# Performance work log

Hardware: AMD Instinct MI355X
Metric: run time of the kernel (lower is better)

The kernel has to match this reference:

```python
import jax, jax.numpy as jnp
import numpy as np

N_NODES = 100000
H_FEATS = 256
N_EDGES = 300000
NUM_CLASSES = 1


def setup_inputs() -> dict:
    key = jax.random.key(0)
    k1, k2, k3, k4, k5 = jax.random.split(key, 5)
    x = jax.random.normal(k1, (N_NODES, H_FEATS), dtype=jnp.float32)
    edge_index = jax.random.randint(k2, (2, N_EDGES), 0, N_NODES, dtype=jnp.int64)
    # MLP params (stored as [in, out] for x @ W + b)
    in1 = 2 * H_FEATS
    W1 = jax.random.normal(k3, (in1, H_FEATS), dtype=jnp.float32) / np.sqrt(in1)
    b1 = jnp.zeros((H_FEATS,), dtype=jnp.float32)
    W2 = jax.random.normal(k4, (H_FEATS, NUM_CLASSES), dtype=jnp.float32) / np.sqrt(H_FEATS)
    b2 = jnp.zeros((NUM_CLASSES,), dtype=jnp.float32)
    return {"x": x, "edge_index": edge_index, "W1": W1, "b1": b1, "W2": W2, "b2": b2}


def reference(x, edge_index, W1, b1, W2, b2):
    # Gather source/dest node embeddings and concat -> [E, 2*h_feats]
    h = jnp.concatenate([x[edge_index[0]], x[edge_index[1]]], axis=-1)
    h = jax.nn.relu(h @ W1 + b1)          # [E, h_feats]
    h = h @ W2 + b2                        # [E, num_classes]
    return jnp.squeeze(h, axis=1)          # [E]
```

## Files before the change

kernel.cpp:

```cpp
#include <hip/hip_runtime.h>
#include <hip/hip_bf16.h>

#define NN 100000
#define H  256
#define NE 300000
#define KOUT 512

typedef __attribute__((ext_vector_type(8))) short short8;
typedef __attribute__((ext_vector_type(8))) unsigned short ushort8v;
typedef __attribute__((ext_vector_type(4))) float f32x4;

__device__ __forceinline__ unsigned short f2bf(float f) {
    unsigned int u = __float_as_uint(f);
    u += 0x7FFFu + ((u >> 16) & 1u);
    return (unsigned short)(u >> 16);
}
__device__ __forceinline__ float bf2f(unsigned short h) {
    return __uint_as_float(((unsigned int)h) << 16);
}
__device__ __forceinline__ int swz(int row, int coloff) {
    return row * 128 + (coloff ^ ((row & 7) << 4));
}

__global__ __launch_bounds__(256) void wprep(const float* __restrict__ W1,
                                             unsigned short* __restrict__ wsB) {
    int gtid = blockIdx.x * 256 + threadIdx.x;
    int t  = gtid >> 10;
    int kg = (gtid >> 7) & 7;
    int n  = gtid & 127;
    int nt = t >> 2, ks = t & 3;
    int krow0 = ks * 64 + kg * 8 + ((nt >= 2) ? 256 : 0);
    int col = (nt & 1) * 128 + n;
    const float* src = W1 + (size_t)krow0 * 256 + col;
    ushort8v p;
    #pragma unroll
    for (int i = 0; i < 8; ++i) p[i] = f2bf(src[(size_t)i * 256]);
    *(ushort8v*)((char*)(wsB + t * 8192) + swz(n, kg * 16)) = p;
}

__global__ __launch_bounds__(256) void gemm_v2(const float* __restrict__ x,
                                               const unsigned short* __restrict__ wsB,
                                               unsigned short* __restrict__ y) {
    __shared__ unsigned short Al[128 * 64];
    __shared__ unsigned short Bl[128 * 64];
    const int tid = threadIdx.x;
    const int logical = ((int)blockIdx.x & 7) * ((int)gridDim.x >> 3) + ((int)blockIdx.x >> 3);
    const int mt = logical >> 2, nt = logical & 3;
    const int m0 = mt * 128;
    const int lane = tid & 63, wid = tid >> 6;
    const int wm = (wid >> 1) * 64, wn = (wid & 1) * 64;
    const int lr = lane & 15, lk = lane >> 4;

    const int arow = tid >> 2;
    const int acolb = (tid & 3) * 16;
    int r0 = m0 + arow;       if (r0 > NN - 1) r0 = NN - 1;
    int r1 = m0 + 64 + arow;  if (r1 > NN - 1) r1 = NN - 1;
    const float* xr0 = x + (size_t)r0 * H + acolb;
    const float* xr1 = x + (size_t)r1 * H + acolb;
    const unsigned short* bt = wsB + nt * 4 * 8192 + tid * 8;

    float4 pA[2][4];
    ushort8v pB[4];

    auto loadA = [&](int ks) {
        const float* s0 = xr0 + ks * 64;
        const float* s1 = xr1 + ks * 64;
        #pragma unroll
        for (int q = 0; q < 4; ++q) pA[0][q] = *(const float4*)(s0 + q * 4);
        #pragma unroll
        for (int q = 0; q < 4; ++q) pA[1][q] = *(const float4*)(s1 + q * 4);
    };
    auto loadB = [&](int ks) {
        const unsigned short* s = bt + ks * 8192;
        #pragma unroll
        for (int u = 0; u < 4; ++u) pB[u] = *(const ushort8v*)(s + u * 2048);
    };
    auto stage = [&]() {
        #pragma unroll
        for (int p = 0; p < 2; ++p) {
            int row = arow + p * 64;
            ushort8v q0, q1;
            q0[0]=f2bf(pA[p][0].x); q0[1]=f2bf(pA[p][0].y); q0[2]=f2bf(pA[p][0].z); q0[3]=f2bf(pA[p][0].w);
            q0[4]=f2bf(pA[p][1].x); q0[5]=f2bf(pA[p][1].y); q0[6]=f2bf(pA[p][1].z); q0[7]=f2bf(pA[p][1].w);
            q1[0]=f2bf(pA[p][2].x); q1[1]=f2bf(pA[p][2].y); q1[2]=f2bf(pA[p][2].z); q1[3]=f2bf(pA[p][2].w);
            q1[4]=f2bf(pA[p][3].x); q1[5]=f2bf(pA[p][3].y); q1[6]=f2bf(pA[p][3].z); q1[7]=f2bf(pA[p][3].w);
            *(ushort8v*)((char*)Al + swz(row, acolb * 2))      = q0;
            *(ushort8v*)((char*)Al + swz(row, acolb * 2 + 16)) = q1;
        }
        #pragma unroll
        for (int u = 0; u < 4; ++u) *(ushort8v*)(Bl + tid * 8 + u * 2048) = pB[u];
    };

    f32x4 acc[4][4] = {};
    loadA(0); loadB(0);
    #pragma unroll
    for (int ks = 0; ks < 4; ++ks) {
        stage();
        __syncthreads();
        if (ks < 3) { loadA(ks + 1); loadB(ks + 1); }
        #pragma unroll
        for (int kk = 0; kk < 64; kk += 32) {
            short8 a[4], b[4];
            const int coloff = kk * 2 + lk * 16;
            #pragma unroll
            for (int mi = 0; mi < 4; ++mi)
                a[mi] = *(const short8*)((const char*)Al + swz(wm + mi * 16 + lr, coloff));
            #pragma unroll
            for (int ni = 0; ni < 4; ++ni)
                b[ni] = *(const short8*)((const char*)Bl + swz(wn + ni * 16 + lr, coloff));
            #pragma unroll
            for (int mi = 0; mi < 4; ++mi)
                #pragma unroll
                for (int ni = 0; ni < 4; ++ni)
                    acc[mi][ni] = __builtin_amdgcn_mfma_f32_16x16x32_bf16(a[mi], b[ni], acc[mi][ni], 0, 0, 0);
        }
        if (ks < 3) {
            asm volatile("s_waitcnt lgkmcnt(0)" ::: "memory");
            __builtin_amdgcn_s_barrier();
            __builtin_amdgcn_sched_barrier(0);
        }
    }
    const int n0 = nt * 128;
    #pragma unroll
    for (int mi = 0; mi < 4; ++mi) {
        #pragma unroll
        for (int ni = 0; ni < 4; ++ni) {
            const int col = n0 + wn + ni * 16 + lr;
            #pragma unroll
            for (int r = 0; r < 4; ++r) {
                const int rowg = m0 + wm + mi * 16 + lk * 4 + r;
                if (rowg < NN) y[(size_t)rowg * KOUT + col] = f2bf(acc[mi][ni][r]);
            }
        }
    }
}

__global__ __launch_bounds__(256) void gemm_v1(const float* __restrict__ x,
                                               const float* __restrict__ W1,
                                               unsigned short* __restrict__ y) {
    __shared__ unsigned short Al[128 * 64];
    __shared__ unsigned short Bl[128 * 64];
    const int tid = threadIdx.x;
    const int bid = blockIdx.x;
    const int mt = bid >> 2, nt = bid & 3;
    const int m0 = mt * 128, n0 = nt * 128;
    const int lane = tid & 63, wid = tid >> 6;
    const int wm = (wid >> 1) * 64, wn = (wid & 1) * 64;
    const int lr = lane & 15, lk = lane >> 4;
    f32x4 acc[4][4] = {};
    for (int ks = 0; ks < 4; ++ks) {
        const int k0 = ks * 64;
        if (ks) __syncthreads();
        #pragma unroll
        for (int pass = 0; pass < 2; ++pass) {
            int f = pass * 4096 + tid * 16;
            int row = f >> 6, col = f & 63;
            int node = m0 + row;
            node = node < NN ? node : NN - 1;
            const float* src = x + (size_t)node * H + k0 + col;
            float4 v0 = *(const float4*)(src + 0);
            float4 v1 = *(const float4*)(src + 4);
            float4 v2 = *(const float4*)(src + 8);
            float4 v3 = *(const float4*)(src + 12);
            ushort8v p0, p1;
            p0[0]=f2bf(v0.x); p0[1]=f2bf(v0.y); p0[2]=f2bf(v0.z); p0[3]=f2bf(v0.w);
            p0[4]=f2bf(v1.x); p0[5]=f2bf(v1.y); p0[6]=f2bf(v1.z); p0[7]=f2bf(v1.w);
            p1[0]=f2bf(v2.x); p1[1]=f2bf(v2.y); p1[2]=f2bf(v2.z); p1[3]=f2bf(v2.w);
            p1[4]=f2bf(v3.x); p1[5]=f2bf(v3.y); p1[6]=f2bf(v3.z); p1[7]=f2bf(v3.w);
            *(ushort8v*)((char*)Al + swz(row, col * 2))      = p0;
            *(ushort8v*)((char*)Al + swz(row, col * 2 + 16)) = p1;
        }
        {
            int j  = tid & 127;
            int kh = tid >> 7;
            int rowbase = (n0 >= 256) ? 256 : 0;
            const float* wp = W1 + (size_t)(k0 + kh * 32 + rowbase) * 256 + (n0 & 255) + j;
            #pragma unroll
            for (int q = 0; q < 4; ++q) {
                ushort8v p;
                #pragma unroll
                for (int i = 0; i < 8; ++i) p[i] = f2bf(wp[(q * 8 + i) * 256]);
                *(ushort8v*)((char*)Bl + swz(j, (kh * 32 + q * 8) * 2)) = p;
            }
        }
        __syncthreads();
        #pragma unroll
        for (int kk = 0; kk < 64; kk += 32) {
            short8 a[4], b[4];
            const int coloff = kk * 2 + lk * 16;
            #pragma unroll
            for (int mi = 0; mi < 4; ++mi)
                a[mi] = *(const short8*)((const char*)Al + swz(wm + mi * 16 + lr, coloff));
            #pragma unroll
            for (int ni = 0; ni < 4; ++ni)
                b[ni] = *(const short8*)((const char*)Bl + swz(wn + ni * 16 + lr, coloff));
            #pragma unroll
            for (int mi = 0; mi < 4; ++mi)
                #pragma unroll
                for (int ni = 0; ni < 4; ++ni)
                    acc[mi][ni] = __builtin_amdgcn_mfma_f32_16x16x32_bf16(a[mi], b[ni], acc[mi][ni], 0, 0, 0);
        }
    }
    #pragma unroll
    for (int mi = 0; mi < 4; ++mi)
        #pragma unroll
        for (int ni = 0; ni < 4; ++ni) {
            const int col = n0 + wn + ni * 16 + lr;
            #pragma unroll
            for (int r = 0; r < 4; ++r) {
                const int rowg = m0 + wm + mi * 16 + lk * 4 + r;
                if (rowg < NN) y[(size_t)rowg * KOUT + col] = f2bf(acc[mi][ni][r]);
            }
        }
}

__global__ __launch_bounds__(256) void edge_v2(const unsigned short* __restrict__ y,
                                               const int* __restrict__ ei,
                                               const float* __restrict__ b1,
                                               const float* __restrict__ W2,
                                               const float* __restrict__ b2,
                                               float* __restrict__ out) {
    const int tid = threadIdx.x;
    const int l32 = tid & 31;
    const int ghw = ((int)(blockIdx.x * blockDim.x) + tid) >> 5;
    const int nhw = ((int)(gridDim.x * blockDim.x)) >> 5;
    const int j = l32 * 8;
    const float4 b01 = *(const float4*)(b1 + j);
    const float4 b23 = *(const float4*)(b1 + j + 4);
    const float4 w01 = *(const float4*)(W2 + j);
    const float4 w23 = *(const float4*)(W2 + j + 4);
    const float bb = b2[0];
    #pragma unroll 2
    for (int e = ghw; e < NE; e += nhw) {
        int s = ei[e], d = ei[NE + e];
        s = s < 0 ? 0 : (s > NN - 1 ? NN - 1 : s);
        d = d < 0 ? 0 : (d > NN - 1 ? NN - 1 : d);
        ushort8v us = *(const ushort8v*)(y + (size_t)s * KOUT + j);
        ushort8v ud = *(const ushort8v*)(y + (size_t)d * KOUT + 256 + j);
        float acc;
        acc  = fmaxf(bf2f(us[0]) + bf2f(ud[0]) + b01.x, 0.f) * w01.x;
        acc += fmaxf(bf2f(us[1]) + bf2f(ud[1]) + b01.y, 0.f) * w01.y;
        acc += fmaxf(bf2f(us[2]) + bf2f(ud[2]) + b01.z, 0.f) * w01.z;
        acc += fmaxf(bf2f(us[3]) + bf2f(ud[3]) + b01.w, 0.f) * w01.w;
        acc += fmaxf(bf2f(us[4]) + bf2f(ud[4]) + b23.x, 0.f) * w23.x;
        acc += fmaxf(bf2f(us[5]) + bf2f(ud[5]) + b23.y, 0.f) * w23.y;
        acc += fmaxf(bf2f(us[6]) + bf2f(ud[6]) + b23.z, 0.f) * w23.z;
        acc += fmaxf(bf2f(us[7]) + bf2f(ud[7]) + b23.w, 0.f) * w23.w;
        #pragma unroll
        for (int off = 16; off > 0; off >>= 1) acc += __shfl_xor(acc, off, 64);
        if (l32 == 0) out[e] = acc + bb;
    }
}

__global__ __launch_bounds__(256) void fused_fallback(const float* __restrict__ x,
                                                      const int* __restrict__ ei,
                                                      const float* __restrict__ W1,
                                                      const float* __restrict__ b1,
                                                      const float* __restrict__ W2,
                                                      const float* __restrict__ b2,
                                                      float* __restrict__ out) {
    __shared__ float xsh[4][512];
    const int lane = threadIdx.x & 63;
    const int wl = threadIdx.x >> 6;
    const int gw = (blockIdx.x * blockDim.x + threadIdx.x) >> 6;
    const int nw = (gridDim.x * blockDim.x) >> 6;
    const int j = lane * 4;
    const float4 bv = *(const float4*)(b1 + j);
    const float4 wv = *(const float4*)(W2 + j);
    const float bb = b2[0];
    for (int e = gw; e < NE; e += nw) {
        int s = ei[e], d = ei[NE + e];
        s = min(max(s, 0), NN - 1);
        d = min(max(d, 0), NN - 1);
        __threadfence_block();
        #pragma unroll
        for (int i = 0; i < 4; ++i) {
            xsh[wl][i * 64 + lane]       = x[(size_t)s * H + i * 64 + lane];
            xsh[wl][256 + i * 64 + lane] = x[(size_t)d * H + i * 64 + lane];
        }
        __threadfence_block();
        float h0 = bv.x, h1 = bv.y, h2 = bv.z, h3 = bv.w;
        for (int k = 0; k < 256; ++k) {
            float xa = xsh[wl][k], xb = xsh[wl][256 + k];
            float4 wa = *(const float4*)(W1 + (size_t)k * 256 + j);
            float4 wb = *(const float4*)(W1 + (size_t)(k + 256) * 256 + j);
            h0 += xa * wa.x + xb * wb.x;
            h1 += xa * wa.y + xb * wb.y;
            h2 += xa * wa.z + xb * wb.z;
            h3 += xa * wa.w + xb * wb.w;
        }
        float acc = fmaxf(h0, 0.f) * wv.x + fmaxf(h1, 0.f) * wv.y +
                    fmaxf(h2, 0.f) * wv.z + fmaxf(h3, 0.f) * wv.w;
        #pragma unroll
        for (int off = 32; off > 0; off >>= 1) acc += __shfl_xor(acc, off, 64);
        if (lane == 0) out[e] = acc + bb;
    }
}

extern "C" void kernel_launch(void* const* d_in, const int* in_sizes, int n_in,
                              void* d_out, int out_size, void* d_ws, size_t ws_size,
                              hipStream_t stream) {
    const float* x  = (const float*)d_in[0];
    const int*   ei = (const int*)d_in[1];
    const float* W1 = (const float*)d_in[2];
    const float* b1 = (const float*)d_in[3];
    const float* W2 = (const float*)d_in[4];
    const float* b2 = (const float*)d_in[5];
    float* out = (float*)d_out;

    const size_t ybytes = (size_t)NN * KOUT * sizeof(unsigned short);
    const size_t wbytes = 16 * 8192 * sizeof(unsigned short);
    const int mtiles = (NN + 127) / 128;

    if (ws_size >= ybytes + wbytes) {
        unsigned short* yb = (unsigned short*)d_ws;
        unsigned short* wb = (unsigned short*)((char*)d_ws + ybytes);
        wprep<<<dim3(64), dim3(256), 0, stream>>>(W1, wb);
        gemm_v2<<<dim3(mtiles * 4), dim3(256), 0, stream>>>(x, wb, yb);
        edge_v2<<<dim3(2048), dim3(256), 0, stream>>>(yb, ei, b1, W2, b2, out);
    } else if (ws_size >= ybytes) {
        unsigned short* yb = (unsigned short*)d_ws;
        gemm_v1<<<dim3(mtiles * 4), dim3(256), 0, stream>>>(x, W1, yb);
        edge_v2<<<dim3(2048), dim3(256), 0, stream>>>(yb, ei, b1, W2, b2, out);
    } else {
        fused_fallback<<<dim3(2048), dim3(256), 0, stream>>>(x, ei, W1, b1, W2, b2, out);
    }
}
```

Baseline: 117.5 us.

## Pre-convert x to swizzled bf16 tiles and load GEMM tiles via global_load_lds

Adds an xprep kernel that converts x to bf16 once, in the pre-swizzled tile layout the GEMM uses. A new gemm_v3 then copies A and B tiles straight into LDS with global_load_lds instead of staging through registers, and drops the software-pipelined prefetch that gemm_v2 had. The GEMM reads half as many bytes for x, but the extra pass writes and re-reads a ~25MB bf16 copy of x, and gemm_v3 no longer overlaps loads with compute. gemm_v1 is removed.

```diff
diff --git a/kernel.cpp b/kernel.cpp
--- a/kernel.cpp
+++ b/kernel.cpp
@@ -5,6 +5,7 @@
 #define H  256
 #define NE 300000
 #define KOUT 512
+#define MTILES 782
 
 typedef __attribute__((ext_vector_type(8))) short short8;
 typedef __attribute__((ext_vector_type(8))) unsigned short ushort8v;
@@ -20,6 +21,11 @@
 }
 __device__ __forceinline__ int swz(int row, int coloff) {
     return row * 128 + (coloff ^ ((row & 7) << 4));
+}
+__device__ __forceinline__ void gload16(const void* g, void* l) {
+    __builtin_amdgcn_global_load_lds((const __attribute__((address_space(1))) void*)g,
+                                     (__attribute__((address_space(3))) void*)l,
+                                     16, 0, 0);
 }
 
 __global__ __launch_bounds__(256) void wprep(const float* __restrict__ W1,
@@ -36,6 +42,82 @@
     #pragma unroll
     for (int i = 0; i < 8; ++i) p[i] = f2bf(src[(size_t)i * 256]);
     *(ushort8v*)((char*)(wsB + t * 8192) + swz(n, kg * 16)) = p;
+}
+
+__global__ __launch_bounds__(256) void xprep(const float* __restrict__ x,
+                                             unsigned short* __restrict__ xb) {
+    int gid = blockIdx.x * 256 + threadIdx.x;
+    int t   = gid >> 10;
+    int r   = (gid >> 3) & 127;
+    int cg  = gid & 7;
+    int mt = t >> 2, ks = t & 3;
+    int node = mt * 128 + r; if (node > NN - 1) node = NN - 1;
+    const float* src = x + (size_t)node * H + ks * 64 + cg * 8;
+    float4 v0 = *(const float4*)(src);
+    float4 v1 = *(const float4*)(src + 4);
+    ushort8v p;
+    p[0]=f2bf(v0.x); p[1]=f2bf(v0.y); p[2]=f2bf(v0.z); p[3]=f2bf(v0.w);
+    p[4]=f2bf(v1.x); p[5]=f2bf(v1.y); p[6]=f2bf(v1.z); p[7]=f2bf(v1.w);
+    *(ushort8v*)((char*)(xb + (size_t)t * 8192) + swz(r, cg * 16)) = p;
+}
+
+__global__ __launch_bounds__(256) void gemm_v3(const unsigned short* __restrict__ xb,
+                                               const unsigned short* __restrict__ wsB,
+                                               unsigned short* __restrict__ y) {
+    __shared__ unsigned short Al[8192];
+    __shared__ unsigned short Bl[8192];
+    const int tid = threadIdx.x;
+    const int logical = ((int)blockIdx.x & 7) * ((int)gridDim.x >> 3) + ((int)blockIdx.x >> 3);
+    const int mt = logical >> 2, nt = logical & 3;
+    const int m0 = mt * 128, n0 = nt * 128;
+    const int lane = tid & 63, wid = tid >> 6;
+    const int wm = (wid >> 1) * 64, wn = (wid & 1) * 64;
+    const int lr = lane & 15, lk = lane >> 4;
+
+    const char* asrc = (const char*)(xb + (size_t)mt * 4 * 8192) + wid * 4096 + lane * 16;
+    const char* bsrc = (const char*)(wsB + nt * 4 * 8192) + wid * 4096 + lane * 16;
+    char* adst = (char*)Al + wid * 4096;
+    char* bdst = (char*)Bl + wid * 4096;
+
+    f32x4 acc[4][4] = {};
+    #pragma unroll
+    for (int ks = 0; ks < 4; ++ks) {
+        if (ks) __syncthreads();
+        #pragma unroll
+        for (int i = 0; i < 4; ++i) {
+            gload16(asrc + ks * 16384 + i * 1024, adst + i * 1024);
+            gload16(bsrc + ks * 16384 + i * 1024, bdst + i * 1024);
+        }
+        __syncthreads();
+        #pragma unroll
+        for (int kk = 0; kk < 64; kk += 32) {
+            short8 a[4], b[4];
+            const int coloff = kk * 2 + lk * 16;
+            #pragma unroll
+            for (int mi = 0; mi < 4; ++mi)
+                a[mi] = *(const short8*)((const char*)Al + swz(wm + mi * 16 + lr, coloff));
+            #pragma unroll
+            for (int ni = 0; ni < 4; ++ni)
+                b[ni] = *(const short8*)((const char*)Bl + swz(wn + ni * 16 + lr, coloff));
+            #pragma unroll
+            for (int mi = 0; mi < 4; ++mi)
+                #pragma unroll
+                for (int ni = 0; ni < 4; ++ni)
+                    acc[mi][ni] = __builtin_amdgcn_mfma_f32_16x16x32_bf16(a[mi], b[ni], acc[mi][ni], 0, 0, 0);
+        }
+    }
+    #pragma unroll
+    for (int mi = 0; mi < 4; ++mi) {
+        #pragma unroll
+        for (int ni = 0; ni < 4; ++ni) {
+            const int col = n0 + wn + ni * 16 + lr;
+            #pragma unroll
+            for (int r = 0; r < 4; ++r) {
+                const int rowg = m0 + wm + mi * 16 + lk * 4 + r;
+                if (rowg < NN) y[(size_t)rowg * KOUT + col] = f2bf(acc[mi][ni][r]);
+            }
+        }
+    }
 }
 
 __global__ __launch_bounds__(256) void gemm_v2(const float* __restrict__ x,
@@ -61,7 +143,6 @@
 
     float4 pA[2][4];
     ushort8v pB[4];
-
     auto loadA = [&](int ks) {
         const float* s0 = xr0 + ks * 64;
         const float* s1 = xr1 + ks * 64;
@@ -121,86 +202,6 @@
         }
     }
     const int n0 = nt * 128;
-    #pragma unroll
-    for (int mi = 0; mi < 4; ++mi) {
-        #pragma unroll
-        for (int ni = 0; ni < 4; ++ni) {
-            const int col = n0 + wn + ni * 16 + lr;
-            #pragma unroll
-            for (int r = 0; r < 4; ++r) {
-                const int rowg = m0 + wm + mi * 16 + lk * 4 + r;
-                if (rowg < NN) y[(size_t)rowg * KOUT + col] = f2bf(acc[mi][ni][r]);
-            }
-        }
-    }
-}
-
-__global__ __launch_bounds__(256) void gemm_v1(const float* __restrict__ x,
-                                               const float* __restrict__ W1,
-                                               unsigned short* __restrict__ y) {
-    __shared__ unsigned short Al[128 * 64];
-    __shared__ unsigned short Bl[128 * 64];
-    const int tid = threadIdx.x;
-    const int bid = blockIdx.x;
-    const int mt = bid >> 2, nt = bid & 3;
-    const int m0 = mt * 128, n0 = nt * 128;
-    const int lane = tid & 63, wid = tid >> 6;
-    const int wm = (wid >> 1) * 64, wn = (wid & 1) * 64;
-    const int lr = lane & 15, lk = lane >> 4;
-    f32x4 acc[4][4] = {};
-    for (int ks = 0; ks < 4; ++ks) {
-        const int k0 = ks * 64;
-        if (ks) __syncthreads();
-        #pragma unroll
-        for (int pass = 0; pass < 2; ++pass) {
-            int f = pass * 4096 + tid * 16;
-            int row = f >> 6, col = f & 63;
-            int node = m0 + row;
-            node = node < NN ? node : NN - 1;
-            const float* src = x + (size_t)node * H + k0 + col;
-            float4 v0 = *(const float4*)(src + 0);
-            float4 v1 = *(const float4*)(src + 4);
-            float4 v2 = *(const float4*)(src + 8);
-            float4 v3 = *(const float4*)(src + 12);
-            ushort8v p0, p1;
-            p0[0]=f2bf(v0.x); p0[1]=f2bf(v0.y); p0[2]=f2bf(v0.z); p0[3]=f2bf(v0.w);
-            p0[4]=f2bf(v1.x); p0[5]=f2bf(v1.y); p0[6]=f2bf(v1.z); p0[7]=f2bf(v1.w);
-            p1[0]=f2bf(v2.x); p1[1]=f2bf(v2.y); p1[2]=f2bf(v2.z); p1[3]=f2bf(v2.w);
-            p1[4]=f2bf(v3.x); p1[5]=f2bf(v3.y); p1[6]=f2bf(v3.z); p1[7]=f2bf(v3.w);
-            *(ushort8v*)((char*)Al + swz(row, col * 2))      = p0;
-            *(ushort8v*)((char*)Al + swz(row, col * 2 + 16)) = p1;
-        }
-        {
-            int j  = tid & 127;
-            int kh = tid >> 7;
-            int rowbase = (n0 >= 256) ? 256 : 0;
-            const float* wp = W1 + (size_t)(k0 + kh * 32 + rowbase) * 256 + (n0 & 255) + j;
-            #pragma unroll
-            for (int q = 0; q < 4; ++q) {
-                ushort8v p;
-                #pragma unroll
-                for (int i = 0; i < 8; ++i) p[i] = f2bf(wp[(q * 8 + i) * 256]);
-                *(ushort8v*)((char*)Bl + swz(j, (kh * 32 + q * 8) * 2)) = p;
-            }
-        }
-        __syncthreads();
-        #pragma unroll
-        for (int kk = 0; kk < 64; kk += 32) {
-            short8 a[4], b[4];
-            const int coloff = kk * 2 + lk * 16;
-            #pragma unroll
-            for (int mi = 0; mi < 4; ++mi)
-                a[mi] = *(const short8*)((const char*)Al + swz(wm + mi * 16 + lr, coloff));
-            #pragma unroll
-            for (int ni = 0; ni < 4; ++ni)
-                b[ni] = *(const short8*)((const char*)Bl + swz(wn + ni * 16 + lr, coloff));
-            #pragma unroll
-            for (int mi = 0; mi < 4; ++mi)
-                #pragma unroll
-                for (int ni = 0; ni < 4; ++ni)
-                    acc[mi][ni] = __builtin_amdgcn_mfma_f32_16x16x32_bf16(a[mi], b[ni], acc[mi][ni], 0, 0, 0);
-        }
-    }
     #pragma unroll
     for (int mi = 0; mi < 4; ++mi)
         #pragma unroll
@@ -281,13 +282,13 @@
         __threadfence_block();
         float h0 = bv.x, h1 = bv.y, h2 = bv.z, h3 = bv.w;
         for (int k = 0; k < 256; ++k) {
-            float xa = xsh[wl][k], xb = xsh[wl][256 + k];
+            float xa = xsh[wl][k], xb2 = xsh[wl][256 + k];
             float4 wa = *(const float4*)(W1 + (size_t)k * 256 + j);
             float4 wb = *(const float4*)(W1 + (size_t)(k + 256) * 256 + j);
-            h0 += xa * wa.x + xb * wb.x;
-            h1 += xa * wa.y + xb * wb.y;
-            h2 += xa * wa.z + xb * wb.z;
-            h3 += xa * wa.w + xb * wb.w;
+            h0 += xa * wa.x + xb2 * wb.x;
+            h1 += xa * wa.y + xb2 * wb.y;
+            h2 += xa * wa.z + xb2 * wb.z;
+            h3 += xa * wa.w + xb2 * wb.w;
         }
         float acc = fmaxf(h0, 0.f) * wv.x + fmaxf(h1, 0.f) * wv.y +
                     fmaxf(h2, 0.f) * wv.z + fmaxf(h3, 0.f) * wv.w;
@@ -308,19 +309,23 @@
     const float* b2 = (const float*)d_in[5];
     float* out = (float*)d_out;
 
-    const size_t ybytes = (size_t)NN * KOUT * sizeof(unsigned short);
-    const size_t wbytes = 16 * 8192 * sizeof(unsigned short);
-    const int mtiles = (NN + 127) / 128;
-
-    if (ws_size >= ybytes + wbytes) {
+    const size_t ybytes  = (size_t)NN * KOUT * sizeof(unsigned short);
+    const size_t xbbytes = (size_t)MTILES * 4 * 16384;
+    const size_t wbytes  = 16 * 8192 * sizeof(unsigned short);
+
+    if (ws_size >= ybytes + xbbytes + wbytes) {
+        unsigned short* yb  = (unsigned short*)d_ws;
+        unsigned short* xbb = (unsigned short*)((char*)d_ws + ybytes);
+        unsigned short* wb  = (unsigned short*)((char*)d_ws + ybytes + xbbytes);
+        wprep<<<dim3(64), dim3(256), 0, stream>>>(W1, wb);
+        xprep<<<dim3(MTILES * 4 * 4), dim3(256), 0, stream>>>(x, xbb);
+        gemm_v3<<<dim3(MTILES * 4), dim3(256), 0, stream>>>(xbb, wb, yb);
+        edge_v2<<<dim3(2048), dim3(256), 0, stream>>>(yb, ei, b1, W2, b2, out);
+    } else if (ws_size >= ybytes + wbytes) {
         unsigned short* yb = (unsigned short*)d_ws;
         unsigned short* wb = (unsigned short*)((char*)d_ws + ybytes);
         wprep<<<dim3(64), dim3(256), 0, stream>>>(W1, wb);
-        gemm_v2<<<dim3(mtiles * 4), dim3(256), 0, stream>>>(x, wb, yb);
-        edge_v2<<<dim3(2048), dim3(256), 0, stream>>>(yb, ei, b1, W2, b2, out);
-    } else if (ws_size >= ybytes) {
-        unsigned short* yb = (unsigned short*)d_ws;
-        gemm_v1<<<dim3(mtiles * 4), dim3(256), 0, stream>>>(x, W1, yb);
+        gemm_v2<<<dim3(MTILES * 4), dim3(256), 0, stream>>>(x, wb, yb);
         edge_v2<<<dim3(2048), dim3(256), 0, stream>>>(yb, ei, b1, W2, b2, out);
     } else {
         fused_fallback<<<dim3(2048), dim3(256), 0, stream>>>(x, ei, W1, b1, W2, b2, out);
```

Result: no change. 119.4 us (+1.6%).
